# Kernel optimization log

Measured on AMD Instinct MI355X. Metric: run time of the kernel, lower is better.

Reference implementation:

```python
import jax, jax.numpy as jnp
import numpy as np

FILTER_LENGTH = 1024
HOP_LENGTH = 512
CUTOFF = FILTER_LENGTH // 2 + 1  # 513
PAD_AMOUNT = FILTER_LENGTH // 2  # 512


def _make_forward_basis():
    # DFT matrix rows (real stacked over imag, up to Nyquist), windowed by periodic Hann.
    fb = np.fft.fft(np.eye(FILTER_LENGTH))
    fb = np.vstack([np.real(fb[:CUTOFF, :]), np.imag(fb[:CUTOFF, :])])  # [1026, 1024]
    n = np.arange(FILTER_LENGTH)
    # scipy get_window('hann', N, fftbins=True) == periodic Hann
    win = 0.5 * (1.0 - np.cos(2.0 * np.pi * n / FILTER_LENGTH))
    basis = (fb * win[None, :]).astype(np.float32)
    return basis[:, None, :]  # [out_ch=1026, in_ch=1, k=1024]


def setup_inputs() -> dict:
    key = jax.random.key(0)
    audio = jax.random.normal(key, (15360000,), dtype=jnp.float32)
    forward_basis = jnp.asarray(_make_forward_basis())
    return {"audio": audio, "forward_basis": forward_basis}


def reference(audio, forward_basis):
    # [L] -> [1, 1, L + 2*pad] with reflect padding
    x = jnp.pad(audio, (PAD_AMOUNT, PAD_AMOUNT), mode="reflect")[None, None, :]
    # Strided conv1d == windowed DFT per frame; output [1, 1026, n_frames]
    ft = jax.lax.conv_general_dilated(
        x,
        forward_basis,
        window_strides=(HOP_LENGTH,),
        padding="VALID",
        dimension_numbers=("NCH", "OIH", "NCH"),
    )
    real = ft[:, :CUTOFF, :]
    imag = ft[:, CUTOFF:, :]
    return real * real + imag * imag  # power spectrum [1, 513, n_frames]
```

## Files before the change

### kernel.cpp

```cpp
#include <hip/hip_runtime.h>

#define L_AUDIO 15360000
#define PADLEN  15361024
#define FRAMES  30001
#define CHP     513
#define NBAS    (1026*1024)

#define BM  256
#define BNP 128
#define BK  64
#define NKT 16
#define NCB 5
#define NFB 118
#define NWG (NFB*NCB)

typedef __attribute__((ext_vector_type(8))) short short8;
typedef __attribute__((ext_vector_type(4))) float f32x4;

__device__ __forceinline__ unsigned short f2bf(float f) {
    unsigned int u = __float_as_uint(f);
    u += 0x7fffu + ((u >> 16) & 1u);
    return (unsigned short)(u >> 16);
}

__global__ __launch_bounds__(256) void prep_pad_k(const float* __restrict__ a,
                                                  unsigned short* __restrict__ pad) {
    long i = (long)blockIdx.x * blockDim.x + threadIdx.x;
    long p0 = i * 4;
    if (p0 >= 512 && p0 + 4 <= 512 + L_AUDIO) {
        const float4 v = *reinterpret_cast<const float4*>(a + (p0 - 512));
        ushort4 o;
        o.x = f2bf(v.x); o.y = f2bf(v.y); o.z = f2bf(v.z); o.w = f2bf(v.w);
        *reinterpret_cast<ushort4*>(pad + p0) = o;
    } else {
        for (int j = 0; j < 4; ++j) {
            long p = p0 + j;
            long src = p - 512;
            if (p < 512) src = 512 - p;
            else if (src >= L_AUDIO) src = 2L*L_AUDIO - 2 - src;
            pad[p] = f2bf(a[src]);
        }
    }
}

__global__ __launch_bounds__(256) void prep_bas_k(const float* __restrict__ b,
                                                  unsigned short* __restrict__ o) {
    long i = (long)blockIdx.x * blockDim.x + threadIdx.x;
    const float4 v = *reinterpret_cast<const float4*>(b + i * 4);
    ushort4 u;
    u.x = f2bf(v.x); u.y = f2bf(v.y); u.z = f2bf(v.z); u.w = f2bf(v.w);
    *reinterpret_cast<ushort4*>(o + i * 4) = u;
}

__global__ __launch_bounds__(512, 2) void stft_gemm(const unsigned short* __restrict__ pad,
                                                    const unsigned short* __restrict__ bas,
                                                    float* __restrict__ out) {
    __shared__ unsigned short lsA[2][BM * BK];
    __shared__ unsigned short lsB[2][BM * BK];

    const int tid  = threadIdx.x;
    const int w    = tid >> 6;
    const int lane = tid & 63;
    const int l15  = lane & 15;
    const int lk   = lane >> 4;
    const int wm   = w >> 2;
    const int wn   = w & 3;

    const int orig = blockIdx.x;
    const int xcd  = orig & 7;
    const int lid  = orig >> 3;
    const int wg   = (xcd < 6 ? xcd * 74 : 6 * 74 + (xcd - 6) * 73) + lid;
    const int fb   = wg / NCB;
    const int cb   = wg - fb * NCB;
    const long t0  = (long)fb * BM;
    const int  c0  = cb * BNP;

    const unsigned short* aS[4];
    const unsigned short* bS[4];
    #pragma unroll
    for (int j = 0; j < 4; ++j) {
        const int c   = j * 512 + tid;
        const int row = c >> 3;
        const int sc  = (c & 7) ^ (row & 7);
        long tf = t0 + row; if (tf > FRAMES - 1) tf = FRAMES - 1;
        aS[j] = pad + tf * 512 + sc * 8;
        const int g = row >> 4;
        int ch = c0 + (g >> 1) * 16 + (row & 15); if (ch > 512) ch = 512;
        const long brow = (g & 1) ? (long)(513 + ch) : (long)ch;
        bS[j] = bas + brow * 1024 + sc * 8;
    }

    f32x4 acc[8][4];
    #pragma unroll
    for (int a = 0; a < 8; ++a)
        #pragma unroll
        for (int b = 0; b < 4; ++b)
            acc[a][b] = (f32x4){0.f, 0.f, 0.f, 0.f};

    const int wmBase = wm * 128;
    const int wnBase = wn * 64;

#define GLD(dst, src) __builtin_amdgcn_global_load_lds( \
        (const __attribute__((address_space(1))) unsigned int*)(src), \
        (__attribute__((address_space(3))) unsigned int*)(dst), 16, 0, 0)

#define LDSREAD(basePtr, r, S) \
    (*reinterpret_cast<const short8*>(reinterpret_cast<const char*>(basePtr) \
        + (r) * 128 + ((((S) * 4 + lk) ^ ((r) & 7)) << 4)))

    #pragma unroll
    for (int j = 0; j < 4; ++j) {
        GLD(&lsA[0][(j * 512 + tid) * 8], aS[j]);
        GLD(&lsB[0][(j * 512 + tid) * 8], bS[j]);
    }

    for (int t = 0; t < NKT; ++t) {
        unsigned short* curA = lsA[t & 1];
        unsigned short* curB = lsB[t & 1];
        unsigned short* nxtA = lsA[(t & 1) ^ 1];
        unsigned short* nxtB = lsB[(t & 1) ^ 1];
        const bool more = (t + 1 < NKT);
        const int ko = (t + 1) * BK;

        if (more) {
            #pragma unroll
            for (int j = 0; j < 4; ++j) {
                GLD(&nxtA[(j * 512 + tid) * 8], aS[j] + ko);
                GLD(&nxtB[(j * 512 + tid) * 8], bS[j] + ko);
            }
            asm volatile("s_waitcnt vmcnt(8)" ::: "memory");
        } else {
            asm volatile("s_waitcnt vmcnt(0)" ::: "memory");
        }
        __builtin_amdgcn_s_barrier();
        asm volatile("" ::: "memory");

        #pragma unroll
        for (int S = 0; S < 2; ++S) {
            short8 bf[4];
            #pragma unroll
            for (int b = 0; b < 4; ++b)
                bf[b] = LDSREAD(curB, wnBase + b * 16 + l15, S);
            #pragma unroll
            for (int mq = 0; mq < 8; ++mq) {
                short8 af = LDSREAD(curA, wmBase + mq * 16 + l15, S);
                #pragma unroll
                for (int b = 0; b < 4; ++b)
                    acc[mq][b] = __builtin_amdgcn_mfma_f32_16x16x32_bf16(
                        af, bf[b], acc[mq][b], 0, 0, 0);
            }
        }

        asm volatile("" ::: "memory");
        __builtin_amdgcn_s_barrier();
        asm volatile("" ::: "memory");
    }

    const int tb = (int)t0 + wmBase;
    #pragma unroll
    for (int a = 0; a < 8; ++a) {
        #pragma unroll
        for (int q = 0; q < 2; ++q) {
            const int ch = c0 + wn * 32 + q * 16 + l15;
            if (ch >= CHP) continue;
            const long ob = (long)ch * FRAMES;
            const int tv = tb + a * 16 + lk * 4;
            const f32x4 re = acc[a][q * 2];
            const f32x4 im = acc[a][q * 2 + 1];
            if (tv + 3 < FRAMES) {
                #pragma unroll
                for (int r = 0; r < 4; ++r)
                    out[ob + tv + r] = re[r] * re[r] + im[r] * im[r];
            } else {
                #pragma unroll
                for (int r = 0; r < 4; ++r)
                    if (tv + r < FRAMES)
                        out[ob + tv + r] = re[r] * re[r] + im[r] * im[r];
            }
        }
    }
}

extern "C" void kernel_launch(void* const* d_in, const int* in_sizes, int n_in,
                              void* d_out, int out_size, void* d_ws, size_t ws_size,
                              hipStream_t stream) {
    const float* audio = (const float*)d_in[0];
    const float* basis = (const float*)d_in[1];
    float* out = (float*)d_out;

    unsigned short* pad = (unsigned short*)d_ws;
    unsigned short* bas = pad + PADLEN;

    prep_pad_k<<<PADLEN / 4 / 256, 256, 0, stream>>>(audio, pad);
    prep_bas_k<<<NBAS / 4 / 256, 256, 0, stream>>>(basis, bas);

    stft_gemm<<<NWG, 512, 0, stream>>>(pad, bas, out);
}
```

Measured before the change: 114.7 us.

## Split Nyquist channel into scalar side blocks, drop fifth channel tile

```diff
diff --git a/kernel.cpp b/kernel.cpp
--- a/kernel.cpp
+++ b/kernel.cpp
@@ -3,16 +3,13 @@
 #define L_AUDIO 15360000
 #define PADLEN  15361024
 #define FRAMES  30001
-#define CHP     513
 #define NBAS    (1026*1024)
 
-#define BM  256
-#define BNP 128
-#define BK  64
-#define NKT 16
-#define NCB 5
-#define NFB 118
-#define NWG (NFB*NCB)
+#define BM   256
+#define BK   64
+#define NKT  16
+#define NGEMM 472
+#define NWG   504
 
 typedef __attribute__((ext_vector_type(8))) short short8;
 typedef __attribute__((ext_vector_type(4))) float f32x4;
@@ -54,11 +51,44 @@
 
 __global__ __launch_bounds__(512, 2) void stft_gemm(const unsigned short* __restrict__ pad,
                                                     const unsigned short* __restrict__ bas,
+                                                    const float* __restrict__ bas32,
                                                     float* __restrict__ out) {
     __shared__ unsigned short lsA[2][BM * BK];
     __shared__ unsigned short lsB[2][BM * BK];
 
-    const int tid  = threadIdx.x;
+    const int tid = threadIdx.x;
+
+    const int bid = blockIdx.x;
+    const int wg  = (bid & 7) * 63 + (bid >> 3);
+
+    if (wg >= NGEMM) {
+        const int k    = wg - NGEMM;
+        const int base = k * 938;
+        const int lim  = (base + 938 < FRAMES) ? base + 938 : FRAMES;
+        const float* br = bas32 + (long)512  * 1024;
+        const float* bi = bas32 + (long)1025 * 1024;
+        float* o512 = out + (long)512 * FRAMES;
+        #pragma unroll
+        for (int rep = 0; rep < 2; ++rep) {
+            const int f = base + rep * 512 + tid;
+            if (f < lim) {
+                const unsigned short* ap = pad + (long)f * 512;
+                float re = 0.f, im = 0.f;
+                for (int n = 0; n < 1024; n += 8) {
+                    short8 a8 = *reinterpret_cast<const short8*>(ap + n);
+                    #pragma unroll
+                    for (int u = 0; u < 8; ++u) {
+                        float av = __uint_as_float(((unsigned)(unsigned short)a8[u]) << 16);
+                        re = fmaf(av, br[n + u], re);
+                        im = fmaf(av, bi[n + u], im);
+                    }
+                }
+                o512[f] = re * re + im * im;
+            }
+        }
+        return;
+    }
+
     const int w    = tid >> 6;
     const int lane = tid & 63;
     const int l15  = lane & 15;
@@ -66,29 +96,22 @@
     const int wm   = w >> 2;
     const int wn   = w & 3;
 
-    const int orig = blockIdx.x;
-    const int xcd  = orig & 7;
-    const int lid  = orig >> 3;
-    const int wg   = (xcd < 6 ? xcd * 74 : 6 * 74 + (xcd - 6) * 73) + lid;
-    const int fb   = wg / NCB;
-    const int cb   = wg - fb * NCB;
-    const long t0  = (long)fb * BM;
-    const int  c0  = cb * BNP;
-
+    const int  fb = wg >> 2;
+    const int  cb = wg & 3;
+    const long t0 = (long)fb * BM;
+    const int  c0 = cb * 128;
+
+    const int sc = (tid & 7) ^ ((tid >> 3) & 7);
     const unsigned short* aS[4];
-    const unsigned short* bS[4];
     #pragma unroll
     for (int j = 0; j < 4; ++j) {
-        const int c   = j * 512 + tid;
-        const int row = c >> 3;
-        const int sc  = (c & 7) ^ (row & 7);
-        long tf = t0 + row; if (tf > FRAMES - 1) tf = FRAMES - 1;
+        long tf = t0 + j * 64 + (tid >> 3);
+        if (tf > FRAMES - 1) tf = FRAMES - 1;
         aS[j] = pad + tf * 512 + sc * 8;
-        const int g = row >> 4;
-        int ch = c0 + (g >> 1) * 16 + (row & 15); if (ch > 512) ch = 512;
-        const long brow = (g & 1) ? (long)(513 + ch) : (long)ch;
-        bS[j] = bas + brow * 1024 + sc * 8;
-    }
+    }
+    const int ch0 = c0 + ((tid >> 8) << 4) + ((tid >> 3) & 15);
+    const long brow0 = ch0 + (((tid >> 7) & 1) ? 513 : 0);
+    const unsigned short* bS0 = bas + brow0 * 1024 + sc * 8;
 
     f32x4 acc[8][4];
     #pragma unroll
@@ -108,52 +131,62 @@
     (*reinterpret_cast<const short8*>(reinterpret_cast<const char*>(basePtr) \
         + (r) * 128 + ((((S) * 4 + lk) ^ ((r) & 7)) << 4)))
 
+#define MCLUST(AF, MQ) do { \
+    __builtin_amdgcn_s_setprio(1); \
+    _Pragma("unroll") for (int b_ = 0; b_ < 4; ++b_) \
+      _Pragma("unroll") for (int m_ = 0; m_ < 4; ++m_) \
+        acc[(MQ)*4+m_][b_] = __builtin_amdgcn_mfma_f32_16x16x32_bf16( \
+            AF[m_], bf[b_], acc[(MQ)*4+m_][b_], 0, 0, 0); \
+    __builtin_amdgcn_s_setprio(0); } while (0)
+
     #pragma unroll
     for (int j = 0; j < 4; ++j) {
-        GLD(&lsA[0][(j * 512 + tid) * 8], aS[j]);
-        GLD(&lsB[0][(j * 512 + tid) * 8], bS[j]);
-    }
+        GLD(&lsA[0][j * 4096 + tid * 8], aS[j]);
+        GLD(&lsB[0][j * 4096 + tid * 8], bS0 + j * 32768);
+    }
+
+    short8 afA[4], afB[4], bf[4];
 
     for (int t = 0; t < NKT; ++t) {
-        unsigned short* curA = lsA[t & 1];
-        unsigned short* curB = lsB[t & 1];
-        unsigned short* nxtA = lsA[(t & 1) ^ 1];
-        unsigned short* nxtB = lsB[(t & 1) ^ 1];
-        const bool more = (t + 1 < NKT);
-        const int ko = (t + 1) * BK;
-
-        if (more) {
+        const int p = t & 1;
+        const unsigned short* curA = lsA[p];
+        const unsigned short* curB = lsB[p];
+
+        __syncthreads();
+
+        #pragma unroll
+        for (int b = 0; b < 4; ++b) bf[b]  = LDSREAD(curB, wnBase + b * 16 + l15, 0);
+        #pragma unroll
+        for (int m = 0; m < 4; ++m) afA[m] = LDSREAD(curA, wmBase + m * 16 + l15, 0);
+        #pragma unroll
+        for (int m = 0; m < 4; ++m) afB[m] = LDSREAD(curA, wmBase + (m + 4) * 16 + l15, 0);
+
+        if (t + 1 < NKT) {
+            const int ko = (t + 1) * BK;
+            unsigned short* nA = lsA[p ^ 1];
+            unsigned short* nB = lsB[p ^ 1];
             #pragma unroll
             for (int j = 0; j < 4; ++j) {
-                GLD(&nxtA[(j * 512 + tid) * 8], aS[j] + ko);
-                GLD(&nxtB[(j * 512 + tid) * 8], bS[j] + ko);
+                GLD(nA + j * 4096 + tid * 8, aS[j] + ko);
+                GLD(nB + j * 4096 + tid * 8, bS0 + j * 32768 + ko);
             }
-            asm volatile("s_waitcnt vmcnt(8)" ::: "memory");
-        } else {
-            asm volatile("s_waitcnt vmcnt(0)" ::: "memory");
-        }
-        __builtin_amdgcn_s_barrier();
-        asm volatile("" ::: "memory");
-
-        #pragma unroll
-        for (int S = 0; S < 2; ++S) {
-            short8 bf[4];
-            #pragma unroll
-            for (int b = 0; b < 4; ++b)
-                bf[b] = LDSREAD(curB, wnBase + b * 16 + l15, S);
-            #pragma unroll
-            for (int mq = 0; mq < 8; ++mq) {
-                short8 af = LDSREAD(curA, wmBase + mq * 16 + l15, S);
-                #pragma unroll
-                for (int b = 0; b < 4; ++b)
-                    acc[mq][b] = __builtin_amdgcn_mfma_f32_16x16x32_bf16(
-                        af, bf[b], acc[mq][b], 0, 0, 0);
-            }
-        }
-
-        asm volatile("" ::: "memory");
-        __builtin_amdgcn_s_barrier();
-        asm volatile("" ::: "memory");
+        }
+        __builtin_amdgcn_sched_barrier(0);
+        MCLUST(afA, 0);
+        __builtin_amdgcn_sched_barrier(0);
+        #pragma unroll
+        for (int m = 0; m < 4; ++m) afA[m] = LDSREAD(curA, wmBase + m * 16 + l15, 1);
+        __builtin_amdgcn_sched_barrier(0);
+        MCLUST(afB, 1);
+        __builtin_amdgcn_sched_barrier(0);
+        #pragma unroll
+        for (int b = 0; b < 4; ++b) bf[b]  = LDSREAD(curB, wnBase + b * 16 + l15, 1);
+        #pragma unroll
+        for (int m = 0; m < 4; ++m) afB[m] = LDSREAD(curA, wmBase + (m + 4) * 16 + l15, 1);
+        __builtin_amdgcn_sched_barrier(0);
+        MCLUST(afA, 0);
+        __builtin_amdgcn_sched_barrier(0);
+        MCLUST(afB, 1);
     }
 
     const int tb = (int)t0 + wmBase;
@@ -162,7 +195,6 @@
         #pragma unroll
         for (int q = 0; q < 2; ++q) {
             const int ch = c0 + wn * 32 + q * 16 + l15;
-            if (ch >= CHP) continue;
             const long ob = (long)ch * FRAMES;
             const int tv = tb + a * 16 + lk * 4;
             const f32x4 re = acc[a][q * 2];
@@ -194,5 +226,5 @@
     prep_pad_k<<<PADLEN / 4 / 256, 256, 0, stream>>>(audio, pad);
     prep_bas_k<<<NBAS / 4 / 256, 256, 0, stream>>>(basis, bas);
 
-    stft_gemm<<<NWG, 512, 0, stream>>>(pad, bas, out);
-}
+    stft_gemm<<<NWG, 512, 0, stream>>>(pad, bas, basis, out);
+}
```

Result: slower. 119.7 us (+4.3%).
